# Performance work log

Hardware: AMD Instinct MI355X
Metric: run time of the kernel (lower is better)

Reference implementation:

```python
import jax, jax.numpy as jnp
import numpy as np

B, T, E = 256, 33, 1024
L = T - 1  # one distinct LSTM per timestep


def setup_inputs() -> dict:
    key = jax.random.key(0)
    k1, k2, k3, k4 = jax.random.split(key, 4)
    scale = 1.0 / np.sqrt(E)  # matches nn.LSTM default uniform init
    return {
        "input_feature_vectors": jax.random.normal(k1, (B, T, E), jnp.float32),
        "target_feature_vector": jax.random.normal(k2, (B, E), jnp.float32),
        "W_ih": jax.random.uniform(k3, (L, 4 * E, E), jnp.float32, -scale, scale),
        "W_hh": jax.random.uniform(k4, (L, 4 * E, E), jnp.float32, -scale, scale),
    }


def _lstm_step(carry, inp):
    h, c = carry                      # [B, E] each
    x_t, w_ih, w_hh = inp             # [B, E], [4E, E], [4E, E]
    gates = x_t @ w_ih.T + h @ w_hh.T  # [B, 4E]; bias=False in the original
    i, f, g, o = jnp.split(gates, 4, axis=-1)  # torch gate order: i, f, g, o
    i = jax.nn.sigmoid(i)
    f = jax.nn.sigmoid(f)
    g = jnp.tanh(g)
    o = jax.nn.sigmoid(o)
    c = f * c + i * g
    h = o * jnp.tanh(c)
    return (h, c), None


def reference(input_feature_vectors, target_feature_vector, W_ih, W_hh):
    x = input_feature_vectors
    b, t, e = x.shape
    h0 = jnp.zeros((b, e), x.dtype)            # h_0 = zeros(1, B, E)
    c0 = x[:, 1, :]                            # c_0 = input[:, 1:2, :].transpose(0,1)
    xs = jnp.swapaxes(x[:, : t - 1, :], 0, 1)  # [T-1, B, E], steps 0..T-2
    (h, c), _ = jax.lax.scan(_lstm_step, (h0, c0), (xs, W_ih, W_hh))
    # output[:, 0, :] of the last step is the final h
    loss = jnp.mean(jnp.abs(h - target_feature_vector))  # L1Loss (mean)
    return loss, h, c
```

## Files before the change

kernel.cpp:

```cpp
#include <hip/hip_runtime.h>
#include <hip/hip_bf16.h>

typedef __attribute__((ext_vector_type(8))) short bf16x8;
typedef __attribute__((ext_vector_type(4))) float f32x4;
typedef __attribute__((ext_vector_type(16))) float f32x16;

static constexpr int BB = 256;
static constexpr int TT = 33;
static constexpr int EE = 1024;
static constexpr int LL = 32;
static constexpr int NG = 4096;

static constexpr int BUF_SZ  = 24576;
static constexpr int A_OFF   = 16384;
static constexpr int NBUF    = 6;
static constexpr int LDS_DYN = 147456;

__device__ __forceinline__ short f2bf(float f) {
  unsigned u = __builtin_bit_cast(unsigned, f);
  u += 0x7fffu + ((u >> 16) & 1u);
  return (short)(u >> 16);
}

__device__ __forceinline__ bf16x8 cvt8(f32x4 a, f32x4 b) {
  bf16x8 r;
  r[0] = f2bf(a[0]); r[1] = f2bf(a[1]); r[2] = f2bf(a[2]); r[3] = f2bf(a[3]);
  r[4] = f2bf(b[0]); r[5] = f2bf(b[1]); r[6] = f2bf(b[2]); r[7] = f2bf(b[3]);
  return r;
}

__device__ __forceinline__ float sigm(float x) { return 1.0f / (1.0f + __expf(-x)); }
__device__ __forceinline__ float tanh_f(float x) { return 1.0f - 2.0f / (__expf(2.0f * x) + 1.0f); }

__global__ __launch_bounds__(256) void lstm_prep(
    const float* __restrict__ x, short* __restrict__ xbf, float* __restrict__ c_io,
    unsigned* __restrict__ flags)
{
  if (blockIdx.x == 0)
    __hip_atomic_store(&flags[(size_t)threadIdx.x * 64], 0u,
                       __ATOMIC_RELAXED, __HIP_MEMORY_SCOPE_AGENT);
  int gth = blockIdx.x * 256 + threadIdx.x;
  int eb  = gth & 127;
  int row = (gth >> 7) & 255;
  int t   = gth >> 15;
  const float* src = x + ((size_t)row * TT + t) * EE + (eb << 3);
  f32x4 lo = *(const f32x4*)src;
  f32x4 hi = *(const f32x4*)(src + 4);
  *(bf16x8*)(xbf + ((size_t)t * BB + row) * EE + (eb << 3)) = cvt8(lo, hi);
  if (t == 1) {
    float* cd = c_io + (size_t)row * EE + (eb << 3);
    *(f32x4*)cd = lo;
    *(f32x4*)(cd + 4) = hi;
  }
}

__global__ __launch_bounds__(512) void lstm_rec(
    const short* __restrict__ xbf,
    const float* __restrict__ Wih,
    const float* __restrict__ Whh,
    short* __restrict__ hroll,
    float* __restrict__ c_io,
    float* __restrict__ h_out,
    unsigned* __restrict__ flags)
{
  extern __shared__ __align__(16) char smem[];

  const int tid  = threadIdx.x;
  const int lane = tid & 63;
  const int wv   = tid >> 6;
  const int ct   = wv & 1;
  const int kh   = wv >> 1;

  const int wg     = blockIdx.x;
  const int xcd    = wg & 7;
  const int jj     = wg >> 3;
  const int rowgrp = jj & 3;
  const int ehi    = jj >> 2;
  const int e0     = (xcd * 8 + ehi) << 4;
  const int row0   = rowgrp << 6;

  size_t wsrc_off[2]; int wdst_off[2];
#pragma unroll
  for (int r = 0; r < 2; ++r) {
    int o = r * 8192 + wv * 1024 + lane * 16;
    int lrow = o >> 8;
    int mwr = ((lrow & 7) << 5) | ((lrow & 8) << 1);
    wsrc_off[r] = (size_t)((lrow >> 4) * EE + e0 + (lrow & 15)) * 4096 + ((o & 255) ^ mwr);
    wdst_off[r] = r * 8192 + wv * 1024;
  }
  size_t asrc_off; int adst_off;
  {
    int o  = wv * 1024 + lane * 16;
    int G  = o >> 4;
    int rp = G >> 4;
    int s  = G & 15;
    int r  = rp * 2 + (s & 1);
    int g  = ((s >> 1) ^ (rp & 7)) & 7;
    asrc_off = (size_t)(row0 + r) * 2048 + g * 16;
    adst_off = A_OFF + o;
  }

  const int wrow = ct * 32 + (lane & 31);
  const int mg   = ((wrow & 7) << 5) | ((wrow & 8) << 1);
  const int kW   = kh * 64 + ((lane >> 5) << 5);
  const int woff_lo = wrow * 256 + (kW ^ mg);
  const int woff_hi = wrow * 256 + ((kW + 16) ^ mg);
  const int arow = lane & 31;
  const int rpA  = arow >> 1;
  const int gkh  = kh * 2 + (lane >> 5);
  const int sA   = (2 * gkh + (arow & 1)) ^ ((rpA & 7) << 1);
  const int aoff0 = rpA * 256 + sA * 16;

  const int er = tid & 63;
  const int ep = tid >> 6;
  float c0r = c_io[(size_t)(row0 + er) * EE + e0 + 2 * ep];
  float c1r = c_io[(size_t)(row0 + er) * EE + e0 + 2 * ep + 1];

  f32x16 acc0{}, acc1{};

  auto stageC = [&](int tt, int cc, int buf) {
    const int p  = cc >> 4;
    const int k0 = (cc & 15) << 6;
    const char* Wt = (const char*)((p ? Whh : Wih) + (size_t)tt * NG * EE);
    const char* At = p ? (const char*)(hroll + (size_t)(tt - 1) * BB * EE)
                       : (const char*)(xbf + (size_t)tt * BB * EE);
    char* dst = smem + buf * BUF_SZ;
#pragma unroll
    for (int r = 0; r < 2; ++r)
      __builtin_amdgcn_global_load_lds(
          (const __attribute__((address_space(1))) unsigned int*)(Wt + wsrc_off[r] + (k0 << 2)),
          (__attribute__((address_space(3))) unsigned int*)(dst + wdst_off[r]), 16, 0, 0);
    __builtin_amdgcn_global_load_lds(
        (const __attribute__((address_space(1))) unsigned int*)(At + asrc_off + (k0 << 1)),
        (__attribute__((address_space(3))) unsigned int*)(dst + adst_off), 16, 0, 0);
  };

  auto compute = [&](int buf) {
    const char* Wb = smem + buf * BUF_SZ;
    const char* Ab = Wb + A_OFF;
    f32x4 wlo = *(const f32x4*)(Wb + woff_lo);
    f32x4 whi = *(const f32x4*)(Wb + woff_hi);
    bf16x8 bfr = cvt8(wlo, whi);
    bf16x8 a0 = *(const bf16x8*)(Ab + aoff0);
    bf16x8 a1 = *(const bf16x8*)(Ab + aoff0 + 4096);
    acc0 = __builtin_amdgcn_mfma_f32_32x32x16_bf16(a0, bfr, acc0, 0, 0, 0);
    acc1 = __builtin_amdgcn_mfma_f32_32x32x16_bf16(a1, bfr, acc1, 0, 0, 0);
  };

  const int rsw = ((lane >> 1) & 3) << 4;
  auto dumpT = [&](float* base, const f32x16& a) {
    char* b = (char*)base + lane * 64;
#pragma unroll
    for (int jq = 0; jq < 4; ++jq) {
      f32x4 v{a[jq * 4 + 0], a[jq * 4 + 1], a[jq * 4 + 2], a[jq * 4 + 3]};
      *(f32x4*)(b + ((jq * 16) ^ rsw)) = v;
    }
  };
  auto addT = [&](const float* base, f32x16& a) {
    const char* b = (const char*)base + lane * 64;
#pragma unroll
    for (int jq = 0; jq < 4; ++jq) {
      f32x4 v = *(const f32x4*)(b + ((jq * 16) ^ rsw));
      a[jq * 4 + 0] += v[0]; a[jq * 4 + 1] += v[1];
      a[jq * 4 + 2] += v[2]; a[jq * 4 + 3] += v[3];
    }
  };

  stageC(0, 0, 0); stageC(0, 1, 1); stageC(0, 2, 2); stageC(0, 3, 3);

  int fb = 0;
  for (int t = 0; t < LL; ++t) {
    const int nch = t ? 32 : 16;
    const int np  = nch >> 1;
    for (int pc = 0; pc < np; ++pc) {
      bool full = (t == LL - 1 && pc == np - 1);
      if (full) asm volatile("s_waitcnt vmcnt(0) lgkmcnt(0)" ::: "memory");
      else      asm volatile("s_waitcnt vmcnt(6) lgkmcnt(0)" ::: "memory");
      __builtin_amdgcn_s_barrier();

      int sc0 = 2 * pc + 4, st = t;
      if (sc0 >= nch) { sc0 -= nch; st = t + 1; }
      bool skip = (st > t && sc0 == 2) || (st >= LL);
      if (!skip) {
        if (st == t && sc0 == 16) {
          if (tid < 64) {
            unsigned fid = (unsigned)((tid & 7) + 8 * rowgrp + 32 * (tid >> 3));
            while (__hip_atomic_load(flags + (size_t)fid * 64,
                                     __ATOMIC_RELAXED, __HIP_MEMORY_SCOPE_AGENT) < (unsigned)t)
              __builtin_amdgcn_s_sleep(1);
          }
          __builtin_amdgcn_s_barrier();
          __builtin_amdgcn_sched_barrier(0);
        }
        stageC(st, sc0,     (fb + 4) % NBUF);
        stageC(st, sc0 + 1, (fb + 5) % NBUF);
      }

      compute(fb);
      compute(fb + 1);
      fb = (fb + 2) % NBUF;
    }

    asm volatile("s_waitcnt lgkmcnt(0)" ::: "memory");
    __builtin_amdgcn_s_barrier();
    char* red = smem + (size_t)((fb + 4) % NBUF) * BUF_SZ;
    auto slotp = [&](int src, int rt) {
      return (float*)(red + (size_t)((src * 2 + ct) * 2 + rt) * 4096);
    };

    if (kh >= 1) { dumpT(slotp(kh - 1, 0), acc0); dumpT(slotp(kh - 1, 1), acc1); }
    asm volatile("s_waitcnt lgkmcnt(0)" ::: "memory");
    __builtin_amdgcn_s_barrier();

    if (kh == 0) {
#pragma unroll
      for (int src = 0; src < 3; ++src) { addT(slotp(src, 0), acc0); addT(slotp(src, 1), acc1); }
      char* gb = red + wrow * 256;
#pragma unroll
      for (int rt = 0; rt < 2; ++rt) {
        const f32x16& a = rt ? acc1 : acc0;
#pragma unroll
        for (int jq = 0; jq < 4; ++jq) {
          int rowb = rt * 128 + jq * 32 + ((lane >> 5) << 4);
          f32x4 v{a[jq * 4 + 0], a[jq * 4 + 1], a[jq * 4 + 2], a[jq * 4 + 3]};
          *(f32x4*)(gb + (rowb ^ mg)) = v;
        }
      }
    }
    acc0 = f32x16{}; acc1 = f32x16{};
    asm volatile("s_waitcnt lgkmcnt(0)" ::: "memory");
    __builtin_amdgcn_s_barrier();

    {
      auto gate = [&](int g, int ee) {
        int wc = g * 16 + ee;
        int swc = ((wc & 7) << 5) | ((wc & 8) << 1);
        return *(const float*)(red + wc * 256 + ((er * 4) ^ swc));
      };
      int e0c = 2 * ep;
      float gi0 = gate(0, e0c), gf0 = gate(1, e0c), gg0 = gate(2, e0c), go0 = gate(3, e0c);
      float gi1 = gate(0, e0c + 1), gf1 = gate(1, e0c + 1), gg1 = gate(2, e0c + 1), go1 = gate(3, e0c + 1);

      c0r = sigm(gf0) * c0r + sigm(gi0) * tanh_f(gg0);
      float h0n = sigm(go0) * tanh_f(c0r);
      c1r = sigm(gf1) * c1r + sigm(gi1) * tanh_f(gg1);
      float h1n = sigm(go1) * tanh_f(c1r);

      if (t == LL - 1) {
        size_t o0 = (size_t)(row0 + er) * EE + e0 + e0c;
        h_out[o0] = h0n;     c_io[o0] = c0r;
        h_out[o0 + 1] = h1n; c_io[o0 + 1] = c1r;
      } else {
        unsigned pv = (unsigned)(unsigned short)f2bf(h0n)
                    | ((unsigned)(unsigned short)f2bf(h1n) << 16);
        __hip_atomic_store(
            (unsigned*)((char*)hroll + ((size_t)t * BB + row0 + er) * 2048 + (size_t)(e0 + e0c) * 2),
            pv, __ATOMIC_RELAXED, __HIP_MEMORY_SCOPE_AGENT);
      }
    }

    if (t < LL - 1) {
      asm volatile("s_waitcnt vmcnt(0)" ::: "memory");
      stageC(t + 1, 2, (fb + 2) % NBUF);
      stageC(t + 1, 3, (fb + 3) % NBUF);
      __builtin_amdgcn_s_barrier();
      if (tid == 0)
        __hip_atomic_store(flags + (size_t)wg * 64, (unsigned)(t + 1),
                           __ATOMIC_RELAXED, __HIP_MEMORY_SCOPE_AGENT);
    }
  }
}

__global__ __launch_bounds__(256) void lstm_loss_part(
    const float* __restrict__ h, const float* __restrict__ tgt, float* __restrict__ partials)
{
  __shared__ float lds[4];
  int tid = threadIdx.x;
  float s = 0.f;
  int base = blockIdx.x * 1024 + tid;
#pragma unroll
  for (int q = 0; q < 4; ++q) {
    int idx = base + (q << 8);
    s += fabsf(h[idx] - tgt[idx]);
  }
#pragma unroll
  for (int off = 32; off > 0; off >>= 1) s += __shfl_down(s, off, 64);
  if ((tid & 63) == 0) lds[tid >> 6] = s;
  __syncthreads();
  if (tid == 0) partials[blockIdx.x] = lds[0] + lds[1] + lds[2] + lds[3];
}

__global__ __launch_bounds__(256) void lstm_loss_fin(
    const float* __restrict__ partials, float* __restrict__ out)
{
  __shared__ float lds[4];
  int tid = threadIdx.x;
  float s = partials[tid];
#pragma unroll
  for (int off = 32; off > 0; off >>= 1) s += __shfl_down(s, off, 64);
  if ((tid & 63) == 0) lds[tid >> 6] = s;
  __syncthreads();
  if (tid == 0) out[0] = (lds[0] + lds[1] + lds[2] + lds[3]) * (1.0f / 262144.0f);
}

extern "C" void kernel_launch(void* const* d_in, const int* in_sizes, int n_in,
                              void* d_out, int out_size, void* d_ws, size_t ws_size,
                              hipStream_t stream) {
  const float* x   = (const float*)d_in[0];
  const float* tgt = (const float*)d_in[1];
  const float* Wih = (const float*)d_in[2];
  const float* Whh = (const float*)d_in[3];

  float* out   = (float*)d_out;
  float* h_out = out + 1;
  float* c_io  = out + 1 + BB * EE;

  short* xbf      = (short*)d_ws;
  short* hroll    = (short*)((char*)xbf + (size_t)LL * BB * EE * 2);
  float* partials = (float*)((char*)hroll + (size_t)LL * BB * EE * 2);
  unsigned* flags = (unsigned*)((char*)partials + 1024);

  static bool attr_done = false;
  if (!attr_done) {
    hipFuncSetAttribute((const void*)lstm_rec,
                        hipFuncAttributeMaxDynamicSharedMemorySize, LDS_DYN);
    attr_done = true;
  }

  lstm_prep<<<4096, 256, 0, stream>>>(x, xbf, c_io, flags);

  {
    const short* xbfA = xbf; const float* WihA = Wih; const float* WhhA = Whh;
    short* hrollA = hroll; float* cA = c_io; float* hA = h_out; unsigned* flagsA = flags;
    void* args[] = {&xbfA, &WihA, &WhhA, &hrollA, &cA, &hA, &flagsA};
    hipError_t e = hipLaunchCooperativeKernel((void*)lstm_rec, dim3(256), dim3(512),
                                              args, LDS_DYN, stream);
    if (e != hipSuccess)
      lstm_rec<<<256, 512, LDS_DYN, stream>>>(xbf, Wih, Whh, hroll, c_io, h_out, flags);
  }

  lstm_loss_part<<<256, 256, 0, stream>>>(h_out, tgt, partials);
  lstm_loss_fin<<<1, 256, 0, stream>>>(partials, out);
}
```

Baseline: 559.2 us.

## Defer LSTM gate epilogue into next timestep's first chunk to overlap with staging

Moves the per-step gate nonlinearity, h store and flag publish out of the end-of-step block and into the first two chunk iterations of the next timestep. It reads the reduced gates from the rotating buffer. The vmcnt(0) wait and the extra barrier before publishing are removed, so staging of the next weights overlaps the epilogue. The risks are a later flag publish, which may delay dependent workgroups spinning on flags, and relying on the reduction buffer not being overwritten before it is read.

```diff
diff --git a/kernel.cpp b/kernel.cpp
--- a/kernel.cpp
+++ b/kernel.cpp
@@ -166,6 +166,12 @@
     }
   };
 
+  auto gateRd = [&](const char* red, int g, int ee) {
+    int wc = g * 16 + ee;
+    int swc = ((wc & 7) << 5) | ((wc & 8) << 1);
+    return *(const float*)(red + wc * 256 + ((er * 4) ^ swc));
+  };
+
   stageC(0, 0, 0); stageC(0, 1, 1); stageC(0, 2, 2); stageC(0, 3, 3);
 
   int fb = 0;
@@ -177,6 +183,32 @@
       if (full) asm volatile("s_waitcnt vmcnt(0) lgkmcnt(0)" ::: "memory");
       else      asm volatile("s_waitcnt vmcnt(6) lgkmcnt(0)" ::: "memory");
       __builtin_amdgcn_s_barrier();
+
+      if (pc == 0 && t > 0) {
+        const char* red = smem + (size_t)((fb + 4) % NBUF) * BUF_SZ;
+        int e0c = 2 * ep;
+        float gi0 = gateRd(red, 0, e0c),     gf0 = gateRd(red, 1, e0c);
+        float gg0 = gateRd(red, 2, e0c),     go0 = gateRd(red, 3, e0c);
+        float gi1 = gateRd(red, 0, e0c + 1), gf1 = gateRd(red, 1, e0c + 1);
+        float gg1 = gateRd(red, 2, e0c + 1), go1 = gateRd(red, 3, e0c + 1);
+        asm volatile("s_waitcnt lgkmcnt(0)" ::: "memory");
+        __builtin_amdgcn_s_barrier();
+
+        c0r = sigm(gf0) * c0r + sigm(gi0) * tanh_f(gg0);
+        float h0n = sigm(go0) * tanh_f(c0r);
+        c1r = sigm(gf1) * c1r + sigm(gi1) * tanh_f(gg1);
+        float h1n = sigm(go1) * tanh_f(c1r);
+        unsigned pv = (unsigned)(unsigned short)f2bf(h0n)
+                    | ((unsigned)(unsigned short)f2bf(h1n) << 16);
+        __hip_atomic_store(
+            (unsigned*)((char*)hroll + ((size_t)(t - 1) * BB + row0 + er) * 2048 + (size_t)(e0 + e0c) * 2),
+            pv, __ATOMIC_RELAXED, __HIP_MEMORY_SCOPE_AGENT);
+      }
+      if (pc == 1 && t > 0) {
+        if (tid == 0)
+          __hip_atomic_store(flags + (size_t)wg * 64, (unsigned)t,
+                             __ATOMIC_RELAXED, __HIP_MEMORY_SCOPE_AGENT);
+      }
 
       int sc0 = 2 * pc + 4, st = t;
       if (sc0 >= nch) { sc0 -= nch; st = t + 1; }
@@ -231,43 +263,28 @@
     asm volatile("s_waitcnt lgkmcnt(0)" ::: "memory");
     __builtin_amdgcn_s_barrier();
 
-    {
-      auto gate = [&](int g, int ee) {
-        int wc = g * 16 + ee;
-        int swc = ((wc & 7) << 5) | ((wc & 8) << 1);
-        return *(const float*)(red + wc * 256 + ((er * 4) ^ swc));
-      };
-      int e0c = 2 * ep;
-      float gi0 = gate(0, e0c), gf0 = gate(1, e0c), gg0 = gate(2, e0c), go0 = gate(3, e0c);
-      float gi1 = gate(0, e0c + 1), gf1 = gate(1, e0c + 1), gg1 = gate(2, e0c + 1), go1 = gate(3, e0c + 1);
-
-      c0r = sigm(gf0) * c0r + sigm(gi0) * tanh_f(gg0);
-      float h0n = sigm(go0) * tanh_f(c0r);
-      c1r = sigm(gf1) * c1r + sigm(gi1) * tanh_f(gg1);
-      float h1n = sigm(go1) * tanh_f(c1r);
-
-      if (t == LL - 1) {
-        size_t o0 = (size_t)(row0 + er) * EE + e0 + e0c;
-        h_out[o0] = h0n;     c_io[o0] = c0r;
-        h_out[o0 + 1] = h1n; c_io[o0 + 1] = c1r;
-      } else {
-        unsigned pv = (unsigned)(unsigned short)f2bf(h0n)
-                    | ((unsigned)(unsigned short)f2bf(h1n) << 16);
-        __hip_atomic_store(
-            (unsigned*)((char*)hroll + ((size_t)t * BB + row0 + er) * 2048 + (size_t)(e0 + e0c) * 2),
-            pv, __ATOMIC_RELAXED, __HIP_MEMORY_SCOPE_AGENT);
-      }
-    }
-
     if (t < LL - 1) {
-      asm volatile("s_waitcnt vmcnt(0)" ::: "memory");
       stageC(t + 1, 2, (fb + 2) % NBUF);
       stageC(t + 1, 3, (fb + 3) % NBUF);
-      __builtin_amdgcn_s_barrier();
-      if (tid == 0)
-        __hip_atomic_store(flags + (size_t)wg * 64, (unsigned)(t + 1),
-                           __ATOMIC_RELAXED, __HIP_MEMORY_SCOPE_AGENT);
-    }
+    }
+  }
+
+  {
+    const char* red = smem + (size_t)((fb + 4) % NBUF) * BUF_SZ;
+    int e0c = 2 * ep;
+    float gi0 = gateRd(red, 0, e0c),     gf0 = gateRd(red, 1, e0c);
+    float gg0 = gateRd(red, 2, e0c),     go0 = gateRd(red, 3, e0c);
+    float gi1 = gateRd(red, 0, e0c + 1), gf1 = gateRd(red, 1, e0c + 1);
+    float gg1 = gateRd(red, 2, e0c + 1), go1 = gateRd(red, 3, e0c + 1);
+
+    c0r = sigm(gf0) * c0r + sigm(gi0) * tanh_f(gg0);
+    float h0n = sigm(go0) * tanh_f(c0r);
+    c1r = sigm(gf1) * c1r + sigm(gi1) * tanh_f(gg1);
+    float h1n = sigm(go1) * tanh_f(c1r);
+
+    size_t o0 = (size_t)(row0 + er) * EE + e0 + e0c;
+    h_out[o0] = h0n;     c_io[o0] = c0r;
+    h_out[o0 + 1] = h1n; c_io[o0 + 1] = c1r;
   }
 }
 
```

Result: slower. 584.4 us (+4.5%).
